# Optimization experiments

Hardware: AMD Instinct MI355X
Metric: run time of the kernel (lower is better)

The kernel has to match this reference:

```python
import jax, jax.numpy as jnp
import numpy as np
from jax import lax

WINDOW_SIZE = 11
SIGMA = 1.5
C1 = 0.01 ** 2
C2 = 0.03 ** 2


def _make_window():
    xs = np.arange(WINDOW_SIZE) - WINDOW_SIZE // 2
    g = np.exp(-(xs.astype(np.float32) ** 2) / (2.0 * SIGMA ** 2))
    g = g / g.sum()
    w2d = np.outer(g, g).astype(np.float32)  # (ws, ws)
    return jnp.asarray(w2d)[None, None, :, :]  # (O=1, I=1, ws, ws)


def _blur(x, window):
    pad = WINDOW_SIZE // 2
    return lax.conv_general_dilated(
        x, window,
        window_strides=(1, 1),
        padding=[(pad, pad), (pad, pad)],
        dimension_numbers=("NCHW", "OIHW", "NCHW"),
    )


def setup_inputs() -> dict:
    key = jax.random.key(0)
    k1, k2 = jax.random.split(key)
    shape = (64, 1, 512, 512)
    img1 = jax.random.uniform(k1, shape, dtype=jnp.float32)
    img2 = jax.random.uniform(k2, shape, dtype=jnp.float32)
    return {"img1": img1, "img2": img2}


def reference(img1, img2):
    window = _make_window()
    mu1 = _blur(img1, window)
    mu2 = _blur(img2, window)
    mu1_sq = mu1 * mu1
    mu2_sq = mu2 * mu2
    mu1_mu2 = mu1 * mu2
    sigma1_sq = _blur(img1 * img1, window) - mu1_sq
    sigma2_sq = _blur(img2 * img2, window) - mu2_sq
    sigma12 = _blur(img1 * img2, window) - mu1_mu2
    ssim_map = ((2.0 * mu1_mu2 + C1) * (2.0 * sigma12 + C2)) / (
        (mu1_sq + mu2_sq + C1) * (sigma1_sq + sigma2_sq + C2)
    )
    return ssim_map.mean()  # size_average=True
```

## Files before the change

kernel.cpp:

```cpp
#include <hip/hip_runtime.h>

#define IMG 512
#define HALO 5
#define BAND 16
#define NB 16
#define RING 28

#define W0 1.0283800e-03f
#define W1 7.5987582e-03f
#define W2 3.6000773e-02f
#define W3 1.0936070e-01f
#define W4 2.1300553e-01f
#define W5 2.6601172e-01f

typedef float f2 __attribute__((ext_vector_type(2)));

__device__ __forceinline__ f2 pkfma(f2 a, f2 b, f2 c) {
    return __builtin_elementwise_fma(a, b, c);
}

#define LGKM_BARRIER() asm volatile("s_waitcnt lgkmcnt(0)\n\ts_barrier" ::: "memory")

__global__ __launch_bounds__(256, 4)
void ssim_main(const float* __restrict__ img1, const float* __restrict__ img2,
               float* __restrict__ part)
{
    const float Wt[11] = {W0,W1,W2,W3,W4,W5,W4,W3,W2,W1,W0};
    constexpr float C1 = 1.0e-4f;
    constexpr float C2 = 9.0e-4f;

    __shared__ float4 sH4[RING][65];
    __shared__ float  sH1[RING][65];
    __shared__ float  sRed[4];

    const int bx     = blockIdx.x;
    const int n      = bx >> 4;
    const int stripe = (bx >> 1) & 7;
    const int half   = bx & 1;
    const int gx0    = stripe << 6;
    const int base   = half << 8;
    const int tid    = threadIdx.x;
    const bool edge  = (stripe == 0) | (stripe == 7);

    const float* __restrict__ base1 = img1 + (size_t)n * IMG * IMG;
    const float* __restrict__ base2 = img2 + (size_t)n * IMG * IMG;

    float acc = 0.0f;

    auto loadRow = [&](int gr, int cg, float4* px, float4* py) {
        const int c0  = cg << 2;
        const int gcb = gx0 + c0;
        const bool rok = ((unsigned)gr < (unsigned)IMG);
        const float4* r1 = (const float4*)(base1 + (ptrdiff_t)gr * IMG + gcb - 8);
        const float4* r2 = (const float4*)(base2 + (ptrdiff_t)gr * IMG + gcb - 8);
        if (!edge && rok) {
            #pragma unroll
            for (int t = 0; t < 5; ++t) { px[t] = r1[t]; py[t] = r2[t]; }
        } else {
            #pragma unroll
            for (int t = 0; t < 5; ++t) {
                int gc = gcb - 8 + (t << 2);
                bool ok = rok && (gc >= 0) && (gc < IMG);
                px[t] = ok ? r1[t] : make_float4(0.f,0.f,0.f,0.f);
                py[t] = ok ? r2[t] : make_float4(0.f,0.f,0.f,0.f);
            }
        }
    };

    auto horizStore = [&](const float4* px, const float4* py, int slot, int cg) {
        const int c0 = cg << 2;
        float X[20], Y[20];
        #pragma unroll
        for (int t = 0; t < 5; ++t) {
            X[4*t+0]=px[t].x; X[4*t+1]=px[t].y; X[4*t+2]=px[t].z; X[4*t+3]=px[t].w;
            Y[4*t+0]=py[t].x; Y[4*t+1]=py[t].y; Y[4*t+2]=py[t].z; Y[4*t+3]=py[t].w;
        }
        f2 s01[4] = {{0,0},{0,0},{0,0},{0,0}};
        f2 s23[4] = {{0,0},{0,0},{0,0},{0,0}};
        float s4[4] = {0,0,0,0};
        #pragma unroll
        for (int j = 3; j <= 16; ++j) {
            f2 pxy = {X[j], Y[j]};
            f2 psq = pxy * pxy;
            float sxy = X[j] * Y[j];
            #pragma unroll
            for (int o = 0; o < 4; ++o) {
                int k = j - 3 - o;
                if (0 <= k && k < 11) {
                    f2 w2 = {Wt[k], Wt[k]};
                    s01[o] = pkfma(w2, pxy, s01[o]);
                    s23[o] = pkfma(w2, psq, s23[o]);
                    s4[o]  = fmaf(Wt[k], sxy, s4[o]);
                }
            }
        }
        #pragma unroll
        for (int o = 0; o < 4; ++o) {
            sH4[slot][c0+o] = make_float4(s01[o].x, s01[o].y, s23[o].x, s23[o].y);
            sH1[slot][c0+o] = s4[o];
        }
    };

    auto vert = [&](int sb) {
        const int wv  = tid >> 6;
        const int col = tid & 63;
        const int d0  = sb + (wv << 2) - HALO;
        f2 a[14], b[14]; float c[14];
        #pragma unroll
        for (int i = 0; i < 14; ++i) {
            int s = d0 + i;
            s += (s < 0)     ? RING : 0;
            s -= (s >= RING) ? RING : 0;
            float4 t4 = sH4[s][col];
            a[i] = f2{t4.x, t4.y};
            b[i] = f2{t4.z, t4.w};
            c[i] = sH1[s][col];
        }
        #pragma unroll
        for (int q = 0; q < 4; ++q) {
            f2 m = {0,0}, e = {0,0}; float e12 = 0.f;
            #pragma unroll
            for (int k = 0; k < 11; ++k) {
                f2 w2 = {Wt[k], Wt[k]};
                m   = pkfma(w2, a[q+k], m);
                e   = pkfma(w2, b[q+k], e);
                e12 = fmaf(Wt[k], c[q+k], e12);
            }
            f2 msq = m * m;
            float mu12 = m.x * m.y;
            f2 g = e - msq;
            float g12 = e12 - mu12;
            float num = (2.0f*mu12 + C1) * (2.0f*g12 + C2);
            float den = (msq.x + msq.y + C1) * (g.x + g.y + C2);
            acc += num * __builtin_amdgcn_rcpf(den);
        }
    };

    for (int task = tid; task < 26 * 16; task += 256) {
        int i  = task >> 4;
        int cg = task & 15;
        int gr = base - HALO + i;
        int slot = (unsigned)(gr + 2*RING) % (unsigned)RING;
        float4 px[5], py[5];
        loadRow(gr, cg, px, py);
        horizStore(px, py, slot, cg);
    }

    int sb = half ? (256 % RING) : 0;
    const int rr = tid >> 4, cg = tid & 15;
    for (int b = 0; b < NB; ++b) {
        float4 px[5], py[5];
        const bool pf = (b + 1 < NB);
        if (pf) loadRow(base + (b << 4) + 21 + rr, cg, px, py);
        LGKM_BARRIER();
        vert(sb);
        LGKM_BARRIER();
        if (pf) {
            int t = sb + 21 + rr;
            t -= (t >= RING) ? RING : 0;
            t -= (t >= RING) ? RING : 0;
            horizStore(px, py, t, cg);
        }
        sb += BAND;
        sb -= (sb >= RING) ? RING : 0;
    }

    #pragma unroll
    for (int off = 32; off > 0; off >>= 1)
        acc += __shfl_down(acc, off, 64);
    if ((tid & 63) == 0) sRed[tid >> 6] = acc;
    LGKM_BARRIER();
    if (tid == 0) part[bx] = sRed[0] + sRed[1] + sRed[2] + sRed[3];
}

__global__ void ssim_finalize(const float* __restrict__ part, float* __restrict__ out)
{
    double s = 0.0;
    const int t = threadIdx.x;
    for (int i = t; i < 1024; i += 64) s += (double)part[i];
    #pragma unroll
    for (int off = 32; off > 0; off >>= 1)
        s += __shfl_down(s, off, 64);
    if (t == 0) out[0] = (float)(s * (1.0 / 16777216.0));
}

extern "C" void kernel_launch(void* const* d_in, const int* in_sizes, int n_in,
                              void* d_out, int out_size, void* d_ws, size_t ws_size,
                              hipStream_t stream)
{
    const float* img1 = (const float*)d_in[0];
    const float* img2 = (const float*)d_in[1];
    float* out  = (float*)d_out;
    float* part = (float*)d_ws;

    ssim_main<<<1024, 256, 0, stream>>>(img1, img2, part);
    ssim_finalize<<<1, 64, 0, stream>>>(part, out);
}
```

Measured before the change: 203.9 us.

## Merge squared sums into one blurred channel and pack shared ring into float4

The SSIM formula only needs sigma1_sq + sigma2_sq, so the kernel now blurs x²+y² as a single channel instead of blurring x² and y² separately. Together with x·y, the intermediate fits in a single float4 per column, which removes the extra scalar shared array and one LDS read per row in the vertical pass. Ring-slot indexing is rebased to avoid negative wraparound, and row pointers are advanced incrementally with a faster unguarded load path for interior rows. Summing the squares before blurring slightly changes floating-point rounding.

```diff
diff --git a/kernel.cpp b/kernel.cpp
--- a/kernel.cpp
+++ b/kernel.cpp
@@ -29,8 +29,7 @@
     constexpr float C1 = 1.0e-4f;
     constexpr float C2 = 9.0e-4f;
 
-    __shared__ float4 sH4[RING][65];
-    __shared__ float  sH1[RING][65];
+    __shared__ float4 sH[RING][65];
     __shared__ float  sRed[4];
 
     const int bx     = blockIdx.x;
@@ -47,23 +46,14 @@
 
     float acc = 0.0f;
 
-    auto loadRow = [&](int gr, int cg, float4* px, float4* py) {
-        const int c0  = cg << 2;
-        const int gcb = gx0 + c0;
-        const bool rok = ((unsigned)gr < (unsigned)IMG);
-        const float4* r1 = (const float4*)(base1 + (ptrdiff_t)gr * IMG + gcb - 8);
-        const float4* r2 = (const float4*)(base2 + (ptrdiff_t)gr * IMG + gcb - 8);
-        if (!edge && rok) {
-            #pragma unroll
-            for (int t = 0; t < 5; ++t) { px[t] = r1[t]; py[t] = r2[t]; }
-        } else {
-            #pragma unroll
-            for (int t = 0; t < 5; ++t) {
-                int gc = gcb - 8 + (t << 2);
-                bool ok = rok && (gc >= 0) && (gc < IMG);
-                px[t] = ok ? r1[t] : make_float4(0.f,0.f,0.f,0.f);
-                py[t] = ok ? r2[t] : make_float4(0.f,0.f,0.f,0.f);
-            }
+    auto loadRowP = [&](const float* r1, const float* r2, bool rok, int gcb,
+                        float4* px, float4* py) {
+        #pragma unroll
+        for (int t = 0; t < 5; ++t) {
+            int gc = gcb - 8 + (t << 2);
+            bool ok = rok && (gc >= 0) && (gc < IMG);
+            px[t] = ok ? ((const float4*)r1)[t] : make_float4(0.f,0.f,0.f,0.f);
+            py[t] = ok ? ((const float4*)r2)[t] : make_float4(0.f,0.f,0.f,0.f);
         }
     };
 
@@ -75,91 +65,107 @@
             X[4*t+0]=px[t].x; X[4*t+1]=px[t].y; X[4*t+2]=px[t].z; X[4*t+3]=px[t].w;
             Y[4*t+0]=py[t].x; Y[4*t+1]=py[t].y; Y[4*t+2]=py[t].z; Y[4*t+3]=py[t].w;
         }
-        f2 s01[4] = {{0,0},{0,0},{0,0},{0,0}};
-        f2 s23[4] = {{0,0},{0,0},{0,0},{0,0}};
-        float s4[4] = {0,0,0,0};
-        #pragma unroll
-        for (int j = 3; j <= 16; ++j) {
-            f2 pxy = {X[j], Y[j]};
-            f2 psq = pxy * pxy;
-            float sxy = X[j] * Y[j];
-            #pragma unroll
-            for (int o = 0; o < 4; ++o) {
-                int k = j - 3 - o;
-                if (0 <= k && k < 11) {
-                    f2 w2 = {Wt[k], Wt[k]};
-                    s01[o] = pkfma(w2, pxy, s01[o]);
-                    s23[o] = pkfma(w2, psq, s23[o]);
-                    s4[o]  = fmaf(Wt[k], sxy, s4[o]);
-                }
-            }
+        f2 xy[14], sp[14];
+        #pragma unroll
+        for (int j = 0; j < 14; ++j) {
+            float x = X[3+j], y = Y[3+j];
+            xy[j] = f2{x, y};
+            sp[j] = f2{fmaf(x, x, y*y), x*y};
         }
         #pragma unroll
         for (int o = 0; o < 4; ++o) {
-            sH4[slot][c0+o] = make_float4(s01[o].x, s01[o].y, s23[o].x, s23[o].y);
-            sH1[slot][c0+o] = s4[o];
-        }
-    };
-
-    auto vert = [&](int sb) {
-        const int wv  = tid >> 6;
-        const int col = tid & 63;
-        const int d0  = sb + (wv << 2) - HALO;
-        f2 a[14], b[14]; float c[14];
-        #pragma unroll
-        for (int i = 0; i < 14; ++i) {
-            int s = d0 + i;
-            s += (s < 0)     ? RING : 0;
-            s -= (s >= RING) ? RING : 0;
-            float4 t4 = sH4[s][col];
-            a[i] = f2{t4.x, t4.y};
-            b[i] = f2{t4.z, t4.w};
-            c[i] = sH1[s][col];
-        }
-        #pragma unroll
-        for (int q = 0; q < 4; ++q) {
-            f2 m = {0,0}, e = {0,0}; float e12 = 0.f;
+            f2 m = {0.f, 0.f}, t2 = {0.f, 0.f};
             #pragma unroll
             for (int k = 0; k < 11; ++k) {
                 f2 w2 = {Wt[k], Wt[k]};
-                m   = pkfma(w2, a[q+k], m);
-                e   = pkfma(w2, b[q+k], e);
-                e12 = fmaf(Wt[k], c[q+k], e12);
-            }
-            f2 msq = m * m;
-            float mu12 = m.x * m.y;
-            f2 g = e - msq;
-            float g12 = e12 - mu12;
-            float num = (2.0f*mu12 + C1) * (2.0f*g12 + C2);
-            float den = (msq.x + msq.y + C1) * (g.x + g.y + C2);
-            acc += num * __builtin_amdgcn_rcpf(den);
+                m  = pkfma(w2, xy[o+k], m);
+                t2 = pkfma(w2, sp[o+k], t2);
+            }
+            sH[slot][c0+o] = make_float4(m.x, m.y, t2.x, t2.y);
         }
     };
 
     for (int task = tid; task < 26 * 16; task += 256) {
-        int i  = task >> 4;
-        int cg = task & 15;
-        int gr = base - HALO + i;
-        int slot = (unsigned)(gr + 2*RING) % (unsigned)RING;
+        int i   = task >> 4;
+        int cg  = task & 15;
+        int gr  = base - HALO + i;
+        int gcb = gx0 + (cg << 2);
+        const float* r1 = base1 + (ptrdiff_t)gr * IMG + gcb - 8;
+        const float* r2 = base2 + (ptrdiff_t)gr * IMG + gcb - 8;
         float4 px[5], py[5];
-        loadRow(gr, cg, px, py);
-        horizStore(px, py, slot, cg);
+        loadRowP(r1, r2, (unsigned)gr < (unsigned)IMG, gcb, px, py);
+        horizStore(px, py, i, cg);
     }
 
-    int sb = half ? (256 % RING) : 0;
-    const int rr = tid >> 4, cg = tid & 15;
+    const int rr  = tid >> 4;
+    const int cgs = tid & 15;
+    const int gcb = gx0 + (cgs << 2);
+    const float* p1 = base1 + (ptrdiff_t)(base + 21 + rr) * IMG + gcb - 8;
+    const float* p2 = base2 + (ptrdiff_t)(base + 21 + rr) * IMG + gcb - 8;
+
+    int sb = 0;
     for (int b = 0; b < NB; ++b) {
         float4 px[5], py[5];
         const bool pf = (b + 1 < NB);
-        if (pf) loadRow(base + (b << 4) + 21 + rr, cg, px, py);
+        if (pf) {
+            const bool rowsafe = (half == 0) | (b < 14);
+            if (rowsafe & (!edge)) {
+                #pragma unroll
+                for (int t = 0; t < 5; ++t) {
+                    px[t] = ((const float4*)p1)[t];
+                    py[t] = ((const float4*)p2)[t];
+                }
+            } else {
+                int gr = base + (b << 4) + 21 + rr;
+                loadRowP(p1, p2, (unsigned)gr < (unsigned)IMG, gcb, px, py);
+            }
+        }
+
         LGKM_BARRIER();
-        vert(sb);
+
+        {
+            const int wv  = __builtin_amdgcn_readfirstlane(tid >> 6);
+            const int col = tid & 63;
+            const int d0  = sb + (wv << 2);
+            f2 a[14], p[14];
+            #pragma unroll
+            for (int i = 0; i < 14; ++i) {
+                int s = d0 + i;
+                s -= (s >= RING) ? RING : 0;
+                s -= (s >= RING) ? RING : 0;
+                float4 q = sH[s][col];
+                a[i] = f2{q.x, q.y};
+                p[i] = f2{q.z, q.w};
+            }
+            #pragma unroll
+            for (int q4 = 0; q4 < 4; ++q4) {
+                f2 m = {0.f,0.f}, tt = {0.f,0.f};
+                #pragma unroll
+                for (int k = 0; k < 11; ++k) {
+                    f2 w2 = {Wt[k], Wt[k]};
+                    m  = pkfma(w2, a[q4+k], m);
+                    tt = pkfma(w2, p[q4+k], tt);
+                }
+                f2 msq     = m * m;
+                float mu12  = m.x * m.y;
+                float musum = msq.x + msq.y;
+                float g12   = tt.y - mu12;
+                float gs    = tt.x - musum;
+                float num = fmaf(2.f, mu12, C1) * fmaf(2.f, g12, C2);
+                float den = (musum + C1) * (gs + C2);
+                acc = fmaf(num, __builtin_amdgcn_rcpf(den), acc);
+            }
+        }
+
         LGKM_BARRIER();
+
         if (pf) {
-            int t = sb + 21 + rr;
+            int t = sb + 26 + rr;
             t -= (t >= RING) ? RING : 0;
             t -= (t >= RING) ? RING : 0;
-            horizStore(px, py, t, cg);
+            horizStore(px, py, t, cgs);
+            p1 += BAND * IMG;
+            p2 += BAND * IMG;
         }
         sb += BAND;
         sb -= (sb >= RING) ? RING : 0;
```

Result: faster. 174.6 us (-14.4%).
